# Kernel tuning notes

Hardware: AMD Instinct MI355X
Metric: run time of the kernel (lower is better)

Reference implementation:

```python
import jax, jax.numpy as jnp
import numpy as np

B, T, J = 8, 1024, 25
D_MODEL, D_STATE, D_CONV, EXPAND = 256, 16, 4, 2
D_INNER = EXPAND * D_MODEL            # 512
DT_RANK = (D_MODEL + 15) // 16        # 16
N_CLASSES = 60


def layernorm(x, g, b, eps=1e-5):
    mu = x.mean(-1, keepdims=True)
    var = ((x - mu) ** 2).mean(-1, keepdims=True)
    return (x - mu) * jax.lax.rsqrt(var + eps) * g + b


def selective_scan(u, delta, A, Bm, Cm, D):
    # u, delta: [b,l,d]; A: [d,n]; Bm, Cm: [b,l,n]; D: [d]
    dA = jnp.exp(delta[..., None] * A)                              # [b,l,d,n]
    dBu = delta[..., None] * Bm[:, :, None, :] * u[..., None]        # [b,l,d,n]

    def step(h, inp):
        dA_t, dBu_t, C_t = inp
        h = dA_t * h + dBu_t                                         # [b,d,n]
        y = jnp.einsum('bdn,bn->bd', h, C_t)
        return h, y

    h0 = jnp.zeros((u.shape[0], u.shape[2], A.shape[1]), u.dtype)
    _, ys = jax.lax.scan(step, h0, (jnp.moveaxis(dA, 1, 0),
                                    jnp.moveaxis(dBu, 1, 0),
                                    jnp.moveaxis(Cm, 1, 0)))
    return jnp.moveaxis(ys, 0, 1) + u * D                            # [b,l,d]


def setup_inputs() -> dict:
    key = jax.random.key(0)
    ks = jax.random.split(key, 12)
    rn = lambda k, s, sc=0.02: jax.random.normal(k, s, jnp.float32) * sc
    A_log = jnp.log(jnp.tile(jnp.arange(1, D_STATE + 1, dtype=jnp.float32), (D_INNER, 1)))
    return {
        'x': jax.random.normal(ks[0], (B, T, J, 3), jnp.float32),
        'embed_w': rn(ks[1], (D_MODEL, J * 9)), 'embed_b': jnp.zeros((D_MODEL,), jnp.float32),
        'pre_g': jnp.ones((D_MODEL,), jnp.float32), 'pre_b': jnp.zeros((D_MODEL,), jnp.float32),
        'in_proj_w': rn(ks[2], (2 * D_INNER, D_MODEL)),
        'conv_w': rn(ks[3], (D_INNER, 1, D_CONV)), 'conv_b': jnp.zeros((D_INNER,), jnp.float32),
        'x_proj_w': rn(ks[4], (DT_RANK + 2 * D_STATE, D_INNER)),
        'dt_proj_w': rn(ks[5], (D_INNER, DT_RANK)), 'dt_proj_b': rn(ks[6], (D_INNER,), 0.1),
        'A_log': A_log, 'D': jnp.ones((D_INNER,), jnp.float32),
        'out_proj_w': rn(ks[7], (D_MODEL, D_INNER)),
        'post_g': jnp.ones((D_MODEL,), jnp.float32), 'post_b': jnp.zeros((D_MODEL,), jnp.float32),
        'fine_w': rn(ks[8], (N_CLASSES, D_MODEL)), 'fine_b': jnp.zeros((N_CLASSES,), jnp.float32),
    }


def reference(x, embed_w, embed_b, pre_g, pre_b, in_proj_w, conv_w, conv_b,
              x_proj_w, dt_proj_w, dt_proj_b, A_log, D, out_proj_w,
              post_g, post_b, fine_w, fine_b):
    b, t = x.shape[0], x.shape[1]
    # --- SkeletonNormalizer: root-center (scale_joints=None) ---
    pos = x[..., :3] - x[:, :, 0:1, :3]                              # [B,T,J,3]
    # --- MotionFeatureBuilder: pos / vel / acc ---
    vel = jnp.concatenate([jnp.zeros_like(pos[:, :1]), pos[:, 1:] - pos[:, :-1]], axis=1)
    acc = jnp.concatenate([jnp.zeros_like(vel[:, :1]), vel[:, 1:] - vel[:, :-1]], axis=1)
    feat = jnp.concatenate([pos, vel, acc], axis=-1).reshape(b, t, -1)  # [B,T,J*9]
    # --- embed ---
    feat = feat @ embed_w.T + embed_b                                # [B,T,D_MODEL]
    # --- Mamba block on pre-norm, residual add ---
    hn = layernorm(feat, pre_g, pre_b)
    xz = hn @ in_proj_w.T                                            # [B,T,2*D_INNER]
    xm, res = jnp.split(xz, 2, axis=-1)
    # depthwise causal conv1d over time
    xm = jax.lax.conv_general_dilated(
        jnp.swapaxes(xm, 1, 2), conv_w, (1,), [(D_CONV - 1, 0)],
        dimension_numbers=('NCH', 'OIH', 'NCH'), feature_group_count=D_INNER)
    xm = jnp.swapaxes(xm + conv_b[None, :, None], 1, 2)              # [B,T,D_INNER]
    xm = jax.nn.silu(xm)
    dbl = xm @ x_proj_w.T                                            # [B,T,DT_RANK+2*D_STATE]
    dt = dbl[..., :DT_RANK]
    Bm = dbl[..., DT_RANK:DT_RANK + D_STATE]
    Cm = dbl[..., DT_RANK + D_STATE:]
    delta = jax.nn.softplus(dt @ dt_proj_w.T + dt_proj_b)            # [B,T,D_INNER]
    A = -jnp.exp(A_log)                                              # [D_INNER,D_STATE]
    y = selective_scan(xm, delta, A, Bm, Cm, D)
    y = y * jax.nn.silu(res)
    y = y @ out_proj_w.T                                             # [B,T,D_MODEL]
    feat = feat + y
    # --- post norm, mean pool, classify ---
    feat = layernorm(feat, post_g, post_b)
    pooled = feat.mean(axis=1)                                       # [B,D_MODEL]
    return pooled @ fine_w.T + fine_b                                # [B,N_CLASSES]
```

## Files before the change

kernel.cpp:

```cpp
#include <hip/hip_runtime.h>
#include <hip/hip_bf16.h>
#include <math.h>

#define Bb 8
#define Tt 1024
#define Jj 25
#define D_MODEL 256
#define D_STATE 16
#define D_CONV 4
#define D_INNER 512
#define DT_RANK 16
#define N_CLASSES 60
#define Mrows (Bb*Tt)
#define NC 64
#define CL 16

typedef unsigned short u16;
using bf16x8 = __attribute__((ext_vector_type(8))) __bf16;
using f32x4  = __attribute__((ext_vector_type(4))) float;

__device__ inline u16 f2bf(float x) {
    unsigned u = __float_as_uint(x);
    unsigned r = (u + 0x7fffu + ((u >> 16) & 1u)) >> 16;
    return (u16)r;
}
__device__ inline float bf2f(u16 h) { return __uint_as_float((unsigned)h << 16); }
__device__ inline void split2(float x, u16& h, u16& l) {
    h = f2bf(x);
    l = f2bf(x - bf2f(h));
}
__device__ inline float softplus_fast(float s) {
    return fmaxf(s, 0.f) + __logf(1.f + __expf(-fabsf(s)));
}
__device__ inline f32x4 mfma3(bf16x8 ah, bf16x8 al, bf16x8 bh, bf16x8 bl, f32x4 c) {
    c = __builtin_amdgcn_mfma_f32_16x16x32_bf16(al, bh, c, 0, 0, 0);
    c = __builtin_amdgcn_mfma_f32_16x16x32_bf16(ah, bl, c, 0, 0, 0);
    c = __builtin_amdgcn_mfma_f32_16x16x32_bf16(ah, bh, c, 0, 0, 0);
    return c;
}

__global__ __launch_bounds__(256) void prep_kernel(
    const float* __restrict__ x, u16* __restrict__ fh, u16* __restrict__ fl,
    const float* __restrict__ ew, const float* __restrict__ iw,
    const float* __restrict__ xw, const float* __restrict__ ow,
    u16* __restrict__ ebh, u16* __restrict__ ebl,
    u16* __restrict__ iph, u16* __restrict__ ipl,
    u16* __restrict__ xph, u16* __restrict__ xpl,
    u16* __restrict__ oph, u16* __restrict__ opl,
    float* __restrict__ blockpart) {
    int blk = blockIdx.x;
    if (blk < Mrows) {
        int r = blk;
        int c = threadIdx.x;
        float v = 0.f;
        if (c < 225) {
            int t = r & (Tt - 1);
            int j = c / 9;
            int cc = c - j * 9;
            int comp = cc % 3;
            int kind = cc / 3;
            auto POS = [&](int dt) -> float {
                const float* p = x + (long)(r - dt) * Jj * 3;
                return p[j * 3 + comp] - p[comp];
            };
            if (kind == 0) v = POS(0);
            else if (kind == 1) v = (t >= 1) ? (POS(0) - POS(1)) : 0.f;
            else {
                if (t >= 2)      v = POS(0) - 2.f * POS(1) + POS(2);
                else if (t == 1) v = POS(0) - POS(1);
                else             v = 0.f;
            }
        }
        u16 h, l;
        split2(v, h, l);
        fh[(long)r * 256 + c] = h;
        fl[(long)r * 256 + c] = l;
    } else if (blk < Mrows + 1888) {
        int i = (blk - Mrows) * 256 + threadIdx.x;
        const float* src; u16 *dh, *dl; int K, kshift, idx;
        if (i < 65536)       { src = ew; dh = ebh; dl = ebl; K = 225; kshift = 8; idx = i; }
        else if (i < 327680) { src = iw; dh = iph; dl = ipl; K = 256; kshift = 8; idx = i - 65536; }
        else if (i < 352256) { src = xw; dh = xph; dl = xpl; K = 512; kshift = 9; idx = i - 327680; }
        else                 { src = ow; dh = oph; dl = opl; K = 512; kshift = 9; idx = i - 352256; }
        int n = idx >> kshift;
        int k = idx & ((1 << kshift) - 1);
        float v = (k < K) ? src[(long)n * K + k] : 0.f;
        u16 h, l;
        split2(v, h, l);
        dh[idx] = h;
        dl[idx] = l;
    } else {
        int i = (blk - Mrows - 1888) * 256 + threadIdx.x;
        blockpart[i] = 0.f;
    }
}

template<int BM, int BN, int EPI>
__global__ __launch_bounds__(256) void gemm_mfma(
    const u16* __restrict__ Ahi, const u16* __restrict__ Alo, int lda,
    const u16* __restrict__ Whi, const u16* __restrict__ Wlo, int ldw,
    const float* __restrict__ bias, const float* __restrict__ resid, int ldr,
    float* __restrict__ C, int ldc, int M, int N, int K)
{
    constexpr int TM = BM / 32;
    constexpr int TN = BN / 32;
    constexpr int SA = 40;
    __shared__ u16 AsH[BM * SA], AsL[BM * SA];
    __shared__ u16 WsH[BN * SA], WsL[BN * SA];
    int tid = threadIdx.x;
    int m0 = blockIdx.y * BM;
    int n0 = blockIdx.x * BN;
    int lane = tid & 63;
    int wave = tid >> 6;
    int wm = wave >> 1, wn = wave & 1;
    int fr = lane & 15, quad = lane >> 4;
    f32x4 acc[TM][TN] = {};

    for (int k0 = 0; k0 < K; k0 += 32) {
        for (int s = tid; s < BM * 4; s += 256) {
            int row = s >> 2, seg = s & 3;
            long off = (long)(m0 + row) * lda + k0 + seg * 8;
            *(uint4*)&AsH[row * SA + seg * 8] = *(const uint4*)(Ahi + off);
            *(uint4*)&AsL[row * SA + seg * 8] = *(const uint4*)(Alo + off);
        }
        for (int s = tid; s < BN * 4; s += 256) {
            int row = s >> 2, seg = s & 3;
            long off = (long)(n0 + row) * ldw + k0 + seg * 8;
            *(uint4*)&WsH[row * SA + seg * 8] = *(const uint4*)(Whi + off);
            *(uint4*)&WsL[row * SA + seg * 8] = *(const uint4*)(Wlo + off);
        }
        __syncthreads();
        bf16x8 aH[TM], aL[TM], bH[TN], bL[TN];
#pragma unroll
        for (int im = 0; im < TM; im++) {
            int r = wm * (BM / 2) + im * 16 + fr;
            aH[im] = *(const bf16x8*)&AsH[r * SA + quad * 8];
            aL[im] = *(const bf16x8*)&AsL[r * SA + quad * 8];
        }
#pragma unroll
        for (int in = 0; in < TN; in++) {
            int r = wn * (BN / 2) + in * 16 + fr;
            bH[in] = *(const bf16x8*)&WsH[r * SA + quad * 8];
            bL[in] = *(const bf16x8*)&WsL[r * SA + quad * 8];
        }
#pragma unroll
        for (int im = 0; im < TM; im++)
#pragma unroll
            for (int in = 0; in < TN; in++)
                acc[im][in] = mfma3(aH[im], aL[im], bH[in], bL[in], acc[im][in]);
        __syncthreads();
    }
#pragma unroll
    for (int im = 0; im < TM; im++) {
#pragma unroll
        for (int in = 0; in < TN; in++) {
#pragma unroll
            for (int reg = 0; reg < 4; reg++) {
                int gm = m0 + wm * (BM / 2) + im * 16 + quad * 4 + reg;
                int gn = n0 + wn * (BN / 2) + in * 16 + fr;
                float v = acc[im][in][reg];
                if (EPI == 1) v += bias[gn];
                if (EPI == 3) v += resid[(long)gm * ldr + gn];
                C[(long)gm * ldc + gn] = v;
            }
        }
    }
}

__global__ __launch_bounds__(256) void ln_kernel(const float* __restrict__ x,
                                                 const float* __restrict__ g,
                                                 const float* __restrict__ b,
                                                 u16* outh, u16* outl) {
    __shared__ float red[256];
    long r = blockIdx.x;
    int d = threadIdx.x;
    float v = x[r * 256 + d];
    red[d] = v;
    __syncthreads();
    for (int s = 128; s > 0; s >>= 1) {
        if (d < s) red[d] += red[d + s];
        __syncthreads();
    }
    float mu = red[0] * (1.f / 256.f);
    __syncthreads();
    float dv = v - mu;
    red[d] = dv * dv;
    __syncthreads();
    for (int s = 128; s > 0; s >>= 1) {
        if (d < s) red[d] += red[d + s];
        __syncthreads();
    }
    float var = red[0] * (1.f / 256.f);
    float o = dv * rsqrtf(var + 1e-5f) * g[d] + b[d];
    u16 h, l;
    split2(o, h, l);
    outh[r * 256 + d] = h;
    outl[r * 256 + d] = l;
}

__global__ __launch_bounds__(256) void ln_pool_kernel(const float* __restrict__ x,
                                                      const float* __restrict__ g,
                                                      const float* __restrict__ b,
                                                      float* __restrict__ bp) {
    __shared__ float red[256];
    long r = blockIdx.x;
    int d = threadIdx.x;
    float v = x[r * 256 + d];
    red[d] = v;
    __syncthreads();
    for (int s = 128; s > 0; s >>= 1) {
        if (d < s) red[d] += red[d + s];
        __syncthreads();
    }
    float mu = red[0] * (1.f / 256.f);
    __syncthreads();
    float dv = v - mu;
    red[d] = dv * dv;
    __syncthreads();
    for (int s = 128; s > 0; s >>= 1) {
        if (d < s) red[d] += red[d + s];
        __syncthreads();
    }
    float var = red[0] * (1.f / 256.f);
    float o = dv * rsqrtf(var + 1e-5f) * g[d] + b[d];
    atomicAdd(&bp[(r >> 6) * 256 + d], o);
}

__global__ __launch_bounds__(256) void conv_xproj_kernel(
    const float* __restrict__ xz,
    const float* __restrict__ cw, const float* __restrict__ cb,
    const u16* __restrict__ Whi, const u16* __restrict__ Wlo,
    u16* __restrict__ xmh, u16* __restrict__ xml,
    float* __restrict__ dbl)
{
    constexpr int SA = 40;
    __shared__ u16 AsH[16 * SA], AsL[16 * SA];
    __shared__ u16 WsH[64 * SA], WsL[64 * SA];
    int tid = threadIdx.x;
    int m0 = blockIdx.x * 16;
    int lane = tid & 63, wave = tid >> 6;
    int fr = lane & 15, quad = lane >> 4;
    f32x4 acc = {};

    if (tid < 64) {
        int wr = 48 + (tid >> 2), seg = tid & 3;
        *(uint4*)&WsH[wr * SA + seg * 8] = make_uint4(0, 0, 0, 0);
        *(uint4*)&WsL[wr * SA + seg * 8] = make_uint4(0, 0, 0, 0);
    }

    int row = tid >> 4;
    int cg  = tid & 15;
    long gr = m0 + row;
    int t = gr & (Tt - 1);
    const float* xzr = xz + gr * 1024;

    for (int k0 = 0; k0 < 512; k0 += 32) {
        int c0 = k0 + cg * 2;
        float2 x0 = *(const float2*)(xzr + c0);
        float2 x1 = (t >= 1) ? *(const float2*)(xzr - 1024 + c0) : make_float2(0, 0);
        float2 x2 = (t >= 2) ? *(const float2*)(xzr - 2048 + c0) : make_float2(0, 0);
        float2 x3 = (t >= 3) ? *(const float2*)(xzr - 3072 + c0) : make_float2(0, 0);
        u16 hh0, ll0, hh1, ll1;
        {
            float4 w = *(const float4*)(cw + (c0 + 0) * 4);
            float a = cb[c0 + 0] + w.w * x0.x + w.z * x1.x + w.y * x2.x + w.x * x3.x;
            float s = a / (1.f + __expf(-a));
            split2(s, hh0, ll0);
            w = *(const float4*)(cw + (c0 + 1) * 4);
            a = cb[c0 + 1] + w.w * x0.y + w.z * x1.y + w.y * x2.y + w.x * x3.y;
            s = a / (1.f + __expf(-a));
            split2(s, hh1, ll1);
        }
        unsigned ph = hh0 | ((unsigned)hh1 << 16);
        unsigned pl = ll0 | ((unsigned)ll1 << 16);
        *(unsigned*)(xmh + gr * 512 + c0) = ph;
        *(unsigned*)(xml + gr * 512 + c0) = pl;
        *(unsigned*)&AsH[row * SA + cg * 2] = ph;
        *(unsigned*)&AsL[row * SA + cg * 2] = pl;
        if (tid < 192) {
            int wr = tid >> 2, seg = tid & 3;
            long off = (long)wr * 512 + k0 + seg * 8;
            *(uint4*)&WsH[wr * SA + seg * 8] = *(const uint4*)(Whi + off);
            *(uint4*)&WsL[wr * SA + seg * 8] = *(const uint4*)(Wlo + off);
        }
        __syncthreads();
        bf16x8 aH = *(const bf16x8*)&AsH[fr * SA + quad * 8];
        bf16x8 aL = *(const bf16x8*)&AsL[fr * SA + quad * 8];
        int wrow = wave * 16 + fr;
        bf16x8 bH = *(const bf16x8*)&WsH[wrow * SA + quad * 8];
        bf16x8 bL = *(const bf16x8*)&WsL[wrow * SA + quad * 8];
        acc = mfma3(aH, aL, bH, bL, acc);
        __syncthreads();
    }
    int gn = wave * 16 + fr;
    if (gn < 48) {
#pragma unroll
        for (int reg = 0; reg < 4; reg++) {
            int gm = m0 + quad * 4 + reg;
            dbl[(long)gm * 48 + gn] = acc[reg];
        }
    }
}

__global__ __launch_bounds__(512) void scan_p1(const float* __restrict__ dbl,
                                               const float* __restrict__ dtw,
                                               const float* __restrict__ dtb,
                                               const u16* __restrict__ xmh,
                                               const u16* __restrict__ xml,
                                               const float* __restrict__ A_log,
                                               float* __restrict__ chunkS,
                                               float* __restrict__ sumdelta) {
    __shared__ float ds[CL * 48];
    int b = blockIdx.x, c = blockIdx.y, d = threadIdx.x;
    long r0 = (long)b * Tt + (long)c * CL;
    for (int i = d; i < CL * 48; i += 512) ds[i] = dbl[r0 * 48 + i];

    float Arow[16];
#pragma unroll
    for (int n = 0; n < 16; n++) Arow[n] = -expf(A_log[d * 16 + n]);
    float4 wd[4];
#pragma unroll
    for (int q = 0; q < 4; q++) wd[q] = *(const float4*)(dtw + d * 16 + q * 4);
    float bdt = dtb[d];
    float S[16];
#pragma unroll
    for (int n = 0; n < 16; n++) S[n] = 0.f;
    float sd = 0.f;
    __syncthreads();

    for (int t = 0; t < CL; t++) {
        const float* row = ds + t * 48;
        float4 t0 = *(const float4*)(row + 0);
        float4 t1 = *(const float4*)(row + 4);
        float4 t2 = *(const float4*)(row + 8);
        float4 t3 = *(const float4*)(row + 12);
        float s = bdt;
        s += t0.x * wd[0].x + t0.y * wd[0].y + t0.z * wd[0].z + t0.w * wd[0].w;
        s += t1.x * wd[1].x + t1.y * wd[1].y + t1.z * wd[1].z + t1.w * wd[1].w;
        s += t2.x * wd[2].x + t2.y * wd[2].y + t2.z * wd[2].z + t2.w * wd[2].w;
        s += t3.x * wd[3].x + t3.y * wd[3].y + t3.z * wd[3].z + t3.w * wd[3].w;
        float dl = softplus_fast(s);
        long r = r0 + t;
        float u = bf2f(xmh[r * 512 + d]) + bf2f(xml[r * 512 + d]);
        float du = dl * u;
        sd += dl;
        float Bn[16];
#pragma unroll
        for (int q = 0; q < 4; q++) {
            float4 bv = *(const float4*)(row + 16 + q * 4);
            Bn[q*4+0] = bv.x; Bn[q*4+1] = bv.y; Bn[q*4+2] = bv.z; Bn[q*4+3] = bv.w;
        }
#pragma unroll
        for (int n = 0; n < 16; n++) {
            float a = __expf(dl * Arow[n]);
            S[n] = a * S[n] + du * Bn[n];
        }
    }
    long base = ((long)(b * NC + c) * 16) * 512 + d;
#pragma unroll
    for (int n = 0; n < 16; n++) chunkS[base + (long)n * 512] = S[n];
    sumdelta[(long)(b * NC + c) * 512 + d] = sd;
}

__global__ __launch_bounds__(256) void scan_combine(float* chunkS,
                                                    const float* __restrict__ sumdelta,
                                                    const float* __restrict__ A_log) {
    int idx = blockIdx.x * 256 + threadIdx.x;
    int d = idx & 511;
    int n = (idx >> 9) & 15;
    int b = idx >> 13;
    float Aval = -expf(A_log[d * 16 + n]);
    float h = 0.f;
    for (int c = 0; c < NC; c++) {
        long si = ((long)(b * NC + c) * 16 + n) * 512 + d;
        float s = chunkS[si];
        float a = __expf(Aval * sumdelta[(long)(b * NC + c) * 512 + d]);
        chunkS[si] = h;
        h = a * h + s;
    }
}

__global__ __launch_bounds__(512) void scan_p2(const float* __restrict__ dbl,
                                               const float* __restrict__ dtw,
                                               const float* __restrict__ dtb,
                                               const u16* xmh, const u16* xml,
                                               const float* __restrict__ xz,
                                               const float* __restrict__ A_log,
                                               const float* __restrict__ Dv,
                                               const float* __restrict__ chunkH,
                                               u16* yh, u16* yl) {
    __shared__ float ds[CL * 48];
    int b = blockIdx.x, c = blockIdx.y, d = threadIdx.x;
    long r0 = (long)b * Tt + (long)c * CL;
    for (int i = d; i < CL * 48; i += 512) ds[i] = dbl[r0 * 48 + i];

    float Arow[16];
#pragma unroll
    for (int n = 0; n < 16; n++) Arow[n] = -expf(A_log[d * 16 + n]);
    float4 wd[4];
#pragma unroll
    for (int q = 0; q < 4; q++) wd[q] = *(const float4*)(dtw + d * 16 + q * 4);
    float bdt = dtb[d];
    float Dd = Dv[d];
    float h[16];
    long base = ((long)(b * NC + c) * 16) * 512 + d;
#pragma unroll
    for (int n = 0; n < 16; n++) h[n] = chunkH[base + (long)n * 512];
    __syncthreads();

    for (int t = 0; t < CL; t++) {
        const float* row = ds + t * 48;
        float4 t0 = *(const float4*)(row + 0);
        float4 t1 = *(const float4*)(row + 4);
        float4 t2 = *(const float4*)(row + 8);
        float4 t3 = *(const float4*)(row + 12);
        float s = bdt;
        s += t0.x * wd[0].x + t0.y * wd[0].y + t0.z * wd[0].z + t0.w * wd[0].w;
        s += t1.x * wd[1].x + t1.y * wd[1].y + t1.z * wd[1].z + t1.w * wd[1].w;
        s += t2.x * wd[2].x + t2.y * wd[2].y + t2.z * wd[2].z + t2.w * wd[2].w;
        s += t3.x * wd[3].x + t3.y * wd[3].y + t3.z * wd[3].z + t3.w * wd[3].w;
        float dl = softplus_fast(s);
        long r = r0 + t;
        float u = bf2f(xmh[r * 512 + d]) + bf2f(xml[r * 512 + d]);
        float res = xz[r * 1024 + 512 + d];
        float du = dl * u;
        float Bn[16], Cn[16];
#pragma unroll
        for (int q = 0; q < 4; q++) {
            float4 bv = *(const float4*)(row + 16 + q * 4);
            float4 cv = *(const float4*)(row + 32 + q * 4);
            Bn[q*4+0] = bv.x; Bn[q*4+1] = bv.y; Bn[q*4+2] = bv.z; Bn[q*4+3] = bv.w;
            Cn[q*4+0] = cv.x; Cn[q*4+1] = cv.y; Cn[q*4+2] = cv.z; Cn[q*4+3] = cv.w;
        }
        float ysum = 0.f;
#pragma unroll
        for (int n = 0; n < 16; n++) {
            float a = __expf(dl * Arow[n]);
            h[n] = a * h[n] + du * Bn[n];
            ysum += h[n] * Cn[n];
        }
        float yy = ysum + u * Dd;
        float sres = res / (1.f + __expf(-res));
        float outv = yy * sres;
        u16 hh, ll;
        split2(outv, hh, ll);
        yh[r * 512 + d] = hh;
        yl[r * 512 + d] = ll;
    }
}

__global__ __launch_bounds__(256) void head_kernel(const float* __restrict__ bp,
                                                   const float* __restrict__ fw,
                                                   const float* __restrict__ fb,
                                                   float* __restrict__ out) {
    __shared__ float pld[256];
    int b = blockIdx.x;
    int d = threadIdx.x;
    float s = 0.f;
#pragma unroll
    for (int i = 0; i < 16; i++)
        s += bp[(long)(b * 16 + i) * 256 + d];
    pld[d] = s;
    __syncthreads();
    if (d < N_CLASSES) {
        float acc = 0.f;
        for (int k = 0; k < 256; k++) acc += pld[k] * fw[d * 256 + k];
        out[b * N_CLASSES + d] = acc * (1.f / (float)Tt) + fb[d];
    }
}

extern "C" void kernel_launch(void* const* d_in, const int* in_sizes, int n_in,
                              void* d_out, int out_size, void* d_ws, size_t ws_size,
                              hipStream_t stream) {
    const float* x         = (const float*)d_in[0];
    const float* embed_w   = (const float*)d_in[1];
    const float* embed_b   = (const float*)d_in[2];
    const float* pre_g     = (const float*)d_in[3];
    const float* pre_b     = (const float*)d_in[4];
    const float* in_proj_w = (const float*)d_in[5];
    const float* conv_w    = (const float*)d_in[6];
    const float* conv_b    = (const float*)d_in[7];
    const float* x_proj_w  = (const float*)d_in[8];
    const float* dt_proj_w = (const float*)d_in[9];
    const float* dt_proj_b = (const float*)d_in[10];
    const float* A_log     = (const float*)d_in[11];
    const float* Dv        = (const float*)d_in[12];
    const float* out_proj_w= (const float*)d_in[13];
    const float* post_g    = (const float*)d_in[14];
    const float* post_b    = (const float*)d_in[15];
    const float* fine_w    = (const float*)d_in[16];
    const float* fine_b    = (const float*)d_in[17];
    float* out = (float*)d_out;
    char* base = (char*)d_ws;

    float* feat     = (float*)(base + 0);
    float* xz       = (float*)(base + 8388608);
    float* chunkS   = (float*)(base + 41943040);
    u16*   xmh      = (u16*)  (base + 58720256);
    u16*   xml      = (u16*)  (base + 67108864);
    u16*   fbh      = (u16*)  (base + 75497472);
    u16*   fbl      = (u16*)  (base + 79691776);
    float* dbl      = (float*)(base + 83886080);
    float* sumdelta = (float*)(base + 85458944);
    float* blockpart= (float*)(base + 86507520);
    u16*   ebh      = (u16*)  (base + 86638592);
    u16*   ebl      = ebh + 65536;
    u16*   iph      = ebl + 65536;
    u16*   ipl      = iph + 262144;
    u16*   xph      = ipl + 262144;
    u16*   xpl      = xph + 24576;
    u16*   oph      = xpl + 24576;
    u16*   opl      = oph + 131072;

    prep_kernel<<<dim3(Mrows + 1888 + 128), dim3(256), 0, stream>>>(
        x, fbh, fbl, embed_w, in_proj_w, x_proj_w, out_proj_w,
        ebh, ebl, iph, ipl, xph, xpl, oph, opl, blockpart);

    gemm_mfma<64,64,1><<<dim3(4, 128), dim3(256), 0, stream>>>(
        fbh, fbl, 256, ebh, ebl, 256, embed_b, nullptr, 0, feat, 256, Mrows, 256, 256);

    ln_kernel<<<dim3(Mrows), dim3(256), 0, stream>>>(feat, pre_g, pre_b, fbh, fbl);

    gemm_mfma<128,64,0><<<dim3(16, 64), dim3(256), 0, stream>>>(
        fbh, fbl, 256, iph, ipl, 256, nullptr, nullptr, 0, xz, 1024, Mrows, 1024, 256);

    conv_xproj_kernel<<<dim3(Mrows / 16), dim3(256), 0, stream>>>(
        xz, conv_w, conv_b, xph, xpl, xmh, xml, dbl);

    scan_p1<<<dim3(Bb, NC), dim3(512), 0, stream>>>(
        dbl, dt_proj_w, dt_proj_b, xmh, xml, A_log, chunkS, sumdelta);
    scan_combine<<<dim3(256), dim3(256), 0, stream>>>(chunkS, sumdelta, A_log);
    scan_p2<<<dim3(Bb, NC), dim3(512), 0, stream>>>(
        dbl, dt_proj_w, dt_proj_b, xmh, xml, xz, A_log, Dv, chunkS, xmh, xml);

    gemm_mfma<64,64,3><<<dim3(4, 128), dim3(256), 0, stream>>>(
        xmh, xml, 512, oph, opl, 512, nullptr, feat, 256, feat, 256, Mrows, 256, 512);

    ln_pool_kernel<<<dim3(Mrows), dim3(256), 0, stream>>>(feat, post_g, post_b, blockpart);

    head_kernel<<<dim3(Bb), dim3(256), 0, stream>>>(blockpart, fine_w, fine_b, out);
}
```

Baseline: 259.2 us.

## Fuse embedding GEMM with feature build and pre-LN, out_proj with post-LN pooling

Builds the embedding features on the fly inside a new full-row GEMM kernel (32 rows × 256 cols per block) that also applies bias and the pre-LayerNorm in registers. A second fused kernel does the out_proj GEMM, residual add, post-LayerNorm and mean-pool atomics, so the separate LN kernels and the feat round trip after out_proj go away. The aim is to cut kernel launches and global memory traffic for feature and feat tensors. In exchange, each block now streams the full 256-column weight tile, so weight reads per row increase and LDS use is larger, and feature construction now runs inside the GEMM loop.

```diff
diff --git a/kernel.cpp b/kernel.cpp
--- a/kernel.cpp
+++ b/kernel.cpp
@@ -40,7 +40,6 @@
 }
 
 __global__ __launch_bounds__(256) void prep_kernel(
-    const float* __restrict__ x, u16* __restrict__ fh, u16* __restrict__ fl,
     const float* __restrict__ ew, const float* __restrict__ iw,
     const float* __restrict__ xw, const float* __restrict__ ow,
     u16* __restrict__ ebh, u16* __restrict__ ebl,
@@ -49,34 +48,8 @@
     u16* __restrict__ oph, u16* __restrict__ opl,
     float* __restrict__ blockpart) {
     int blk = blockIdx.x;
-    if (blk < Mrows) {
-        int r = blk;
-        int c = threadIdx.x;
-        float v = 0.f;
-        if (c < 225) {
-            int t = r & (Tt - 1);
-            int j = c / 9;
-            int cc = c - j * 9;
-            int comp = cc % 3;
-            int kind = cc / 3;
-            auto POS = [&](int dt) -> float {
-                const float* p = x + (long)(r - dt) * Jj * 3;
-                return p[j * 3 + comp] - p[comp];
-            };
-            if (kind == 0) v = POS(0);
-            else if (kind == 1) v = (t >= 1) ? (POS(0) - POS(1)) : 0.f;
-            else {
-                if (t >= 2)      v = POS(0) - 2.f * POS(1) + POS(2);
-                else if (t == 1) v = POS(0) - POS(1);
-                else             v = 0.f;
-            }
-        }
-        u16 h, l;
-        split2(v, h, l);
-        fh[(long)r * 256 + c] = h;
-        fl[(long)r * 256 + c] = l;
-    } else if (blk < Mrows + 1888) {
-        int i = (blk - Mrows) * 256 + threadIdx.x;
+    if (blk < 1888) {
+        int i = blk * 256 + threadIdx.x;
         const float* src; u16 *dh, *dl; int K, kshift, idx;
         if (i < 65536)       { src = ew; dh = ebh; dl = ebl; K = 225; kshift = 8; idx = i; }
         else if (i < 327680) { src = iw; dh = iph; dl = ipl; K = 256; kshift = 8; idx = i - 65536; }
@@ -90,8 +63,282 @@
         dh[idx] = h;
         dl[idx] = l;
     } else {
-        int i = (blk - Mrows - 1888) * 256 + threadIdx.x;
+        int i = (blk - 1888) * 256 + threadIdx.x;
         blockpart[i] = 0.f;
+    }
+}
+
+__global__ __launch_bounds__(256) void embed_ln_kernel(
+    const float* __restrict__ x,
+    const u16* __restrict__ Whi, const u16* __restrict__ Wlo,
+    const float* __restrict__ bias,
+    const float* __restrict__ g, const float* __restrict__ b,
+    float* __restrict__ feat, u16* __restrict__ hnh, u16* __restrict__ hnl)
+{
+    constexpr int BM = 32, SW = 40;
+    __shared__ u16 AsH[BM * SW], AsL[BM * SW];
+    __shared__ u16 WsH[256 * SW], WsL[256 * SW];
+    __shared__ float red[BM * 4];
+    __shared__ float mu_s[BM], rs_s[BM];
+    int tid = threadIdx.x;
+    int m0 = blockIdx.x * BM;
+    int lane = tid & 63, wave = tid >> 6;
+    int fr = lane & 15, quad = lane >> 4;
+    f32x4 acc[2][4] = {};
+
+    for (int k0 = 0; k0 < 256; k0 += 32) {
+        for (int s = tid; s < BM * 32; s += 256) {
+            int row = s >> 5;
+            int c = k0 + (s & 31);
+            float v = 0.f;
+            if (c < 225) {
+                long r = m0 + row;
+                int t = (int)(r & (Tt - 1));
+                int j = c / 9;
+                int cc = c - j * 9;
+                int comp = cc % 3;
+                int kind = cc / 3;
+                const float* pr = x + r * (Jj * 3);
+                auto POS = [&](int dt) -> float {
+                    const float* p = pr - dt * (Jj * 3);
+                    return p[j * 3 + comp] - p[comp];
+                };
+                if (kind == 0) v = POS(0);
+                else if (kind == 1) v = (t >= 1) ? (POS(0) - POS(1)) : 0.f;
+                else {
+                    if (t >= 2)      v = POS(0) - 2.f * POS(1) + POS(2);
+                    else if (t == 1) v = POS(0) - POS(1);
+                    else             v = 0.f;
+                }
+            }
+            u16 h, l;
+            split2(v, h, l);
+            AsH[row * SW + (s & 31)] = h;
+            AsL[row * SW + (s & 31)] = l;
+        }
+        for (int s = tid; s < 1024; s += 256) {
+            int n = s >> 2, seg = s & 3;
+            long off = (long)n * 256 + k0 + seg * 8;
+            *(uint4*)&WsH[n * SW + seg * 8] = *(const uint4*)(Whi + off);
+            *(uint4*)&WsL[n * SW + seg * 8] = *(const uint4*)(Wlo + off);
+        }
+        __syncthreads();
+        bf16x8 aH[2], aL[2], bH[4], bL[4];
+#pragma unroll
+        for (int im = 0; im < 2; im++) {
+            int r = im * 16 + fr;
+            aH[im] = *(const bf16x8*)&AsH[r * SW + quad * 8];
+            aL[im] = *(const bf16x8*)&AsL[r * SW + quad * 8];
+        }
+#pragma unroll
+        for (int in = 0; in < 4; in++) {
+            int n = wave * 64 + in * 16 + fr;
+            bH[in] = *(const bf16x8*)&WsH[n * SW + quad * 8];
+            bL[in] = *(const bf16x8*)&WsL[n * SW + quad * 8];
+        }
+#pragma unroll
+        for (int im = 0; im < 2; im++)
+#pragma unroll
+            for (int in = 0; in < 4; in++)
+                acc[im][in] = mfma3(aH[im], aL[im], bH[in], bL[in], acc[im][in]);
+        __syncthreads();
+    }
+
+    float bias_c[4], g_c[4], b_c[4];
+#pragma unroll
+    for (int in = 0; in < 4; in++) {
+        int gn = wave * 64 + in * 16 + fr;
+        bias_c[in] = bias[gn];
+        g_c[in] = g[gn];
+        b_c[in] = b[gn];
+    }
+#pragma unroll
+    for (int im = 0; im < 2; im++)
+#pragma unroll
+        for (int in = 0; in < 4; in++)
+#pragma unroll
+            for (int reg = 0; reg < 4; reg++) {
+                float v = acc[im][in][reg] + bias_c[in];
+                acc[im][in][reg] = v;
+                int gm = m0 + im * 16 + quad * 4 + reg;
+                int gn = wave * 64 + in * 16 + fr;
+                feat[(long)gm * 256 + gn] = v;
+            }
+#pragma unroll
+    for (int im = 0; im < 2; im++)
+#pragma unroll
+        for (int reg = 0; reg < 4; reg++) {
+            float p = acc[im][0][reg] + acc[im][1][reg] + acc[im][2][reg] + acc[im][3][reg];
+            p += __shfl_xor(p, 1);
+            p += __shfl_xor(p, 2);
+            p += __shfl_xor(p, 4);
+            p += __shfl_xor(p, 8);
+            if (fr == 0) red[(im * 16 + quad * 4 + reg) * 4 + wave] = p;
+        }
+    __syncthreads();
+    if (tid < BM)
+        mu_s[tid] = (red[tid * 4] + red[tid * 4 + 1] + red[tid * 4 + 2] + red[tid * 4 + 3]) * (1.f / 256.f);
+    __syncthreads();
+#pragma unroll
+    for (int im = 0; im < 2; im++)
+#pragma unroll
+        for (int reg = 0; reg < 4; reg++) {
+            int rl = im * 16 + quad * 4 + reg;
+            float m = mu_s[rl];
+            float d0 = acc[im][0][reg] - m, d1 = acc[im][1][reg] - m;
+            float d2 = acc[im][2][reg] - m, d3 = acc[im][3][reg] - m;
+            float p = d0 * d0 + d1 * d1 + d2 * d2 + d3 * d3;
+            p += __shfl_xor(p, 1);
+            p += __shfl_xor(p, 2);
+            p += __shfl_xor(p, 4);
+            p += __shfl_xor(p, 8);
+            if (fr == 0) red[rl * 4 + wave] = p;
+        }
+    __syncthreads();
+    if (tid < BM) {
+        float v = (red[tid * 4] + red[tid * 4 + 1] + red[tid * 4 + 2] + red[tid * 4 + 3]) * (1.f / 256.f);
+        rs_s[tid] = rsqrtf(v + 1e-5f);
+    }
+    __syncthreads();
+#pragma unroll
+    for (int im = 0; im < 2; im++)
+#pragma unroll
+        for (int in = 0; in < 4; in++)
+#pragma unroll
+            for (int reg = 0; reg < 4; reg++) {
+                int rl = im * 16 + quad * 4 + reg;
+                int gm = m0 + rl;
+                int gn = wave * 64 + in * 16 + fr;
+                float o = (acc[im][in][reg] - mu_s[rl]) * rs_s[rl] * g_c[in] + b_c[in];
+                u16 hh, ll;
+                split2(o, hh, ll);
+                hnh[(long)gm * 256 + gn] = hh;
+                hnl[(long)gm * 256 + gn] = ll;
+            }
+}
+
+__global__ __launch_bounds__(256) void outproj_ln_pool_kernel(
+    const u16* __restrict__ Ahi, const u16* __restrict__ Alo,
+    const u16* __restrict__ Whi, const u16* __restrict__ Wlo,
+    const float* __restrict__ resid,
+    const float* __restrict__ g, const float* __restrict__ b,
+    float* __restrict__ bp)
+{
+    constexpr int BM = 32, SW = 40;
+    __shared__ u16 AsH[BM * SW], AsL[BM * SW];
+    __shared__ u16 WsH[256 * SW], WsL[256 * SW];
+    __shared__ float red[BM * 4];
+    __shared__ float mu_s[BM], rs_s[BM];
+    int tid = threadIdx.x;
+    int m0 = blockIdx.x * BM;
+    int lane = tid & 63, wave = tid >> 6;
+    int fr = lane & 15, quad = lane >> 4;
+    f32x4 acc[2][4] = {};
+
+    for (int k0 = 0; k0 < 512; k0 += 32) {
+        if (tid < 128) {
+            int row = tid >> 2, seg = tid & 3;
+            long off = (long)(m0 + row) * 512 + k0 + seg * 8;
+            *(uint4*)&AsH[row * SW + seg * 8] = *(const uint4*)(Ahi + off);
+            *(uint4*)&AsL[row * SW + seg * 8] = *(const uint4*)(Alo + off);
+        }
+        for (int s = tid; s < 1024; s += 256) {
+            int n = s >> 2, seg = s & 3;
+            long off = (long)n * 512 + k0 + seg * 8;
+            *(uint4*)&WsH[n * SW + seg * 8] = *(const uint4*)(Whi + off);
+            *(uint4*)&WsL[n * SW + seg * 8] = *(const uint4*)(Wlo + off);
+        }
+        __syncthreads();
+        bf16x8 aH[2], aL[2], bH[4], bL[4];
+#pragma unroll
+        for (int im = 0; im < 2; im++) {
+            int r = im * 16 + fr;
+            aH[im] = *(const bf16x8*)&AsH[r * SW + quad * 8];
+            aL[im] = *(const bf16x8*)&AsL[r * SW + quad * 8];
+        }
+#pragma unroll
+        for (int in = 0; in < 4; in++) {
+            int n = wave * 64 + in * 16 + fr;
+            bH[in] = *(const bf16x8*)&WsH[n * SW + quad * 8];
+            bL[in] = *(const bf16x8*)&WsL[n * SW + quad * 8];
+        }
+#pragma unroll
+        for (int im = 0; im < 2; im++)
+#pragma unroll
+            for (int in = 0; in < 4; in++)
+                acc[im][in] = mfma3(aH[im], aL[im], bH[in], bL[in], acc[im][in]);
+        __syncthreads();
+    }
+
+    float g_c[4], b_c[4];
+#pragma unroll
+    for (int in = 0; in < 4; in++) {
+        int gn = wave * 64 + in * 16 + fr;
+        g_c[in] = g[gn];
+        b_c[in] = b[gn];
+    }
+#pragma unroll
+    for (int im = 0; im < 2; im++)
+#pragma unroll
+        for (int in = 0; in < 4; in++)
+#pragma unroll
+            for (int reg = 0; reg < 4; reg++) {
+                int gm = m0 + im * 16 + quad * 4 + reg;
+                int gn = wave * 64 + in * 16 + fr;
+                acc[im][in][reg] += resid[(long)gm * 256 + gn];
+            }
+#pragma unroll
+    for (int im = 0; im < 2; im++)
+#pragma unroll
+        for (int reg = 0; reg < 4; reg++) {
+            float p = acc[im][0][reg] + acc[im][1][reg] + acc[im][2][reg] + acc[im][3][reg];
+            p += __shfl_xor(p, 1);
+            p += __shfl_xor(p, 2);
+            p += __shfl_xor(p, 4);
+            p += __shfl_xor(p, 8);
+            if (fr == 0) red[(im * 16 + quad * 4 + reg) * 4 + wave] = p;
+        }
+    __syncthreads();
+    if (tid < BM)
+        mu_s[tid] = (red[tid * 4] + red[tid * 4 + 1] + red[tid * 4 + 2] + red[tid * 4 + 3]) * (1.f / 256.f);
+    __syncthreads();
+#pragma unroll
+    for (int im = 0; im < 2; im++)
+#pragma unroll
+        for (int reg = 0; reg < 4; reg++) {
+            int rl = im * 16 + quad * 4 + reg;
+            float m = mu_s[rl];
+            float d0 = acc[im][0][reg] - m, d1 = acc[im][1][reg] - m;
+            float d2 = acc[im][2][reg] - m, d3 = acc[im][3][reg] - m;
+            float p = d0 * d0 + d1 * d1 + d2 * d2 + d3 * d3;
+            p += __shfl_xor(p, 1);
+            p += __shfl_xor(p, 2);
+            p += __shfl_xor(p, 4);
+            p += __shfl_xor(p, 8);
+            if (fr == 0) red[rl * 4 + wave] = p;
+        }
+    __syncthreads();
+    if (tid < BM) {
+        float v = (red[tid * 4] + red[tid * 4 + 1] + red[tid * 4 + 2] + red[tid * 4 + 3]) * (1.f / 256.f);
+        rs_s[tid] = rsqrtf(v + 1e-5f);
+    }
+    __syncthreads();
+#pragma unroll
+    for (int in = 0; in < 4; in++) {
+        float cs = 0.f;
+#pragma unroll
+        for (int im = 0; im < 2; im++)
+#pragma unroll
+            for (int reg = 0; reg < 4; reg++) {
+                int rl = im * 16 + quad * 4 + reg;
+                cs += (acc[im][in][reg] - mu_s[rl]) * rs_s[rl] * g_c[in] + b_c[in];
+            }
+        cs += __shfl_xor(cs, 16);
+        cs += __shfl_xor(cs, 32);
+        if (quad == 0) {
+            int gn = wave * 64 + in * 16 + fr;
+            atomicAdd(&bp[(long)(m0 >> 6) * 256 + gn], cs);
+        }
     }
 }
 
@@ -165,65 +412,6 @@
             }
         }
     }
-}
-
-__global__ __launch_bounds__(256) void ln_kernel(const float* __restrict__ x,
-                                                 const float* __restrict__ g,
-                                                 const float* __restrict__ b,
-                                                 u16* outh, u16* outl) {
-    __shared__ float red[256];
-    long r = blockIdx.x;
-    int d = threadIdx.x;
-    float v = x[r * 256 + d];
-    red[d] = v;
-    __syncthreads();
-    for (int s = 128; s > 0; s >>= 1) {
-        if (d < s) red[d] += red[d + s];
-        __syncthreads();
-    }
-    float mu = red[0] * (1.f / 256.f);
-    __syncthreads();
-    float dv = v - mu;
-    red[d] = dv * dv;
-    __syncthreads();
-    for (int s = 128; s > 0; s >>= 1) {
-        if (d < s) red[d] += red[d + s];
-        __syncthreads();
-    }
-    float var = red[0] * (1.f / 256.f);
-    float o = dv * rsqrtf(var + 1e-5f) * g[d] + b[d];
-    u16 h, l;
-    split2(o, h, l);
-    outh[r * 256 + d] = h;
-    outl[r * 256 + d] = l;
-}
-
-__global__ __launch_bounds__(256) void ln_pool_kernel(const float* __restrict__ x,
-                                                      const float* __restrict__ g,
-                                                      const float* __restrict__ b,
-                                                      float* __restrict__ bp) {
-    __shared__ float red[256];
-    long r = blockIdx.x;
-    int d = threadIdx.x;
-    float v = x[r * 256 + d];
-    red[d] = v;
-    __syncthreads();
-    for (int s = 128; s > 0; s >>= 1) {
-        if (d < s) red[d] += red[d + s];
-        __syncthreads();
-    }
-    float mu = red[0] * (1.f / 256.f);
-    __syncthreads();
-    float dv = v - mu;
-    red[d] = dv * dv;
-    __syncthreads();
-    for (int s = 128; s > 0; s >>= 1) {
-        if (d < s) red[d] += red[d + s];
-        __syncthreads();
-    }
-    float var = red[0] * (1.f / 256.f);
-    float o = dv * rsqrtf(var + 1e-5f) * g[d] + b[d];
-    atomicAdd(&bp[(r >> 6) * 256 + d], o);
 }
 
 __global__ __launch_bounds__(256) void conv_xproj_kernel(
@@ -512,14 +700,12 @@
     u16*   oph      = xpl + 24576;
     u16*   opl      = oph + 131072;
 
-    prep_kernel<<<dim3(Mrows + 1888 + 128), dim3(256), 0, stream>>>(
-        x, fbh, fbl, embed_w, in_proj_w, x_proj_w, out_proj_w,
+    prep_kernel<<<dim3(1888 + 128), dim3(256), 0, stream>>>(
+        embed_w, in_proj_w, x_proj_w, out_proj_w,
         ebh, ebl, iph, ipl, xph, xpl, oph, opl, blockpart);
 
-    gemm_mfma<64,64,1><<<dim3(4, 128), dim3(256), 0, stream>>>(
-        fbh, fbl, 256, ebh, ebl, 256, embed_b, nullptr, 0, feat, 256, Mrows, 256, 256);
-
-    ln_kernel<<<dim3(Mrows), dim3(256), 0, stream>>>(feat, pre_g, pre_b, fbh, fbl);
+    embed_ln_kernel<<<dim3(Mrows / 32), dim3(256), 0, stream>>>(
+        x, ebh, ebl, embed_b, pre_g, pre_b, feat, fbh, fbl);
 
     gemm_mfma<128,64,0><<<dim3(16, 64), dim3(256), 0, stream>>>(
         fbh, fbl, 256, iph, ipl, 256, nullptr, nullptr, 0, xz, 1024, Mrows, 1024, 256);
@@ -533,10 +719,8 @@
     scan_p2<<<dim3(Bb, NC), dim3(512), 0, stream>>>(
         dbl, dt_proj_w, dt_proj_b, xmh, xml, xz, A_log, Dv, chunkS, xmh, xml);
 
-    gemm_mfma<64,64,3><<<dim3(4, 128), dim3(256), 0, stream>>>(
-        xmh, xml, 512, oph, opl, 512, nullptr, feat, 256, feat, 256, Mrows, 256, 512);
-
-    ln_pool_kernel<<<dim3(Mrows), dim3(256), 0, stream>>>(feat, post_g, post_b, blockpart);
+    outproj_ln_pool_kernel<<<dim3(Mrows / 32), dim3(256), 0, stream>>>(
+        xmh, xml, oph, opl, feat, post_g, post_b, blockpart);
 
     head_kernel<<<dim3(Bb), dim3(256), 0, stream>>>(blockpart, fine_w, fine_b, out);
 }
```

New measurement: 267.4 us. 1.03x slower.
